# Optimization experiments

Measured on AMD Instinct MI355X. Metric: run time of the kernel, lower is better.

Reference implementation:

```python
import jax, jax.numpy as jnp
import numpy as np

DIM = 1024
NUM_HEADS = 16
HEAD_DIM = DIM // NUM_HEADS
HIDDEN = 2 * DIM  # swiglu hidden


def rotate_half(x):
    x1, x2 = jnp.split(x, 2, axis=-1)
    return jnp.concatenate((-x2, x1), axis=-1)


def setup_inputs() -> dict:
    key = jax.random.key(0)
    ks = jax.random.split(key, 9)
    s = lambda fan_in: 1.0 / np.sqrt(fan_in)
    x = jax.random.normal(ks[0], (4, 2048, DIM), dtype=jnp.float32)
    qkv_w = jax.random.uniform(ks[1], (3 * DIM, DIM), minval=-s(DIM), maxval=s(DIM))
    proj_w = jax.random.uniform(ks[2], (DIM, DIM), minval=-s(DIM), maxval=s(DIM))
    proj_b = jax.random.uniform(ks[3], (DIM,), minval=-s(DIM), maxval=s(DIM))
    w1_w = jax.random.uniform(ks[4], (HIDDEN, DIM), minval=-s(DIM), maxval=s(DIM))
    w1_b = jnp.zeros((HIDDEN,), jnp.float32)
    w2_w = jax.random.uniform(ks[5], (HIDDEN, DIM), minval=-s(DIM), maxval=s(DIM))
    w2_b = jnp.zeros((HIDDEN,), jnp.float32)
    w3_w = jax.random.uniform(ks[6], (DIM, HIDDEN), minval=-s(HIDDEN), maxval=s(HIDDEN))
    w3_b = jnp.zeros((DIM,), jnp.float32)
    return {"x": x, "qkv_w": qkv_w, "proj_w": proj_w, "proj_b": proj_b,
            "w1_w": w1_w, "w1_b": w1_b, "w2_w": w2_w, "w2_b": w2_b,
            "w3_w": w3_w, "w3_b": w3_b}


def reference(x, qkv_w, proj_w, proj_b, w1_w, w1_b, w2_w, w2_b, w3_w, w3_b):
    B, N, C = x.shape
    H, D = NUM_HEADS, HEAD_DIM
    scale = D ** -0.5
    # QKV projection (no bias)
    qkv = jnp.einsum('bnc,fc->bnf', x, qkv_w).reshape(B, N, 3, H, D)
    qkv = jnp.transpose(qkv, (2, 0, 3, 1, 4))  # [3, B, H, N, D]
    q, k, v = qkv[0], qkv[1], qkv[2]
    # Rotary embeddings
    inv_freq = 1.0 / (10000.0 ** (jnp.arange(0, D, 2, dtype=jnp.float32) / D))
    t = jnp.arange(N, dtype=jnp.float32)
    freqs = jnp.einsum('i,j->ij', t, inv_freq)
    emb = jnp.concatenate((freqs, freqs), axis=-1)[None, None]  # [1,1,N,D]
    cos, sin = jnp.cos(emb), jnp.sin(emb)
    q = q * cos + rotate_half(q) * sin
    k = k * cos + rotate_half(k) * sin
    # Attention (non-causal, as in source)
    attn = jnp.einsum('bhnd,bhmd->bhnm', q, k) * scale
    attn = jax.nn.softmax(attn, axis=-1)
    out = jnp.einsum('bhnm,bhmd->bhnd', attn, v)
    out = jnp.transpose(out, (0, 2, 1, 3)).reshape(B, N, C)
    out = jnp.einsum('bnc,fc->bnf', out, proj_w) + proj_b
    # SwiGLU MLP
    x1 = jnp.einsum('bnc,fc->bnf', out, w1_w) + w1_b
    x2 = jnp.einsum('bnc,fc->bnf', out, w2_w) + w2_b
    hidden = jax.nn.silu(x1) * x2
    return jnp.einsum('bnh,fh->bnf', hidden, w3_w) + w3_b
```

## Files before the change

### kernel.cpp

```cpp
#include <hip/hip_runtime.h>
#include <hip/hip_bf16.h>
#include <math.h>


#define SEQ     2048
#define BATCH   4
#define NH      16
#define CDIM    1024
#define MROWS   8192

typedef __bf16 bf16x8 __attribute__((ext_vector_type(8)));
typedef float  floatx4 __attribute__((ext_vector_type(4)));
typedef float  floatx16 __attribute__((ext_vector_type(16)));
typedef unsigned int u32;

__device__ __forceinline__ unsigned short f2bf(float f) {
    __bf16 h = (__bf16)f;
    return __builtin_bit_cast(unsigned short, h);
}
__device__ __forceinline__ float fexp2(float x) {
    float r; asm("v_exp_f32 %0, %1" : "=v"(r) : "v"(x)); return r;
}
__device__ __forceinline__ float frcp(float x) {
    float r; asm("v_rcp_f32 %0, %1" : "=v"(r) : "v"(x)); return r;
}
__device__ __forceinline__ u32 cvtpk(float lo, float hi) {
    u32 w; asm("v_cvt_pk_bf16_f32 %0, %1, %2" : "=v"(w) : "v"(lo), "v"(hi));
    return w;
}
__device__ __forceinline__ floatx4 mfma16(bf16x8 a, bf16x8 b, floatx4 c) {
    return __builtin_amdgcn_mfma_f32_16x16x32_bf16(a, b, c, 0, 0, 0);
}
__device__ __forceinline__ floatx16 mfma32(bf16x8 a, bf16x8 b, floatx16 c) {
    return __builtin_amdgcn_mfma_f32_32x32x16_bf16(a, b, c, 0, 0, 0);
}
__device__ __forceinline__ void gld16(void* lds, const void* g) {
    __builtin_amdgcn_global_load_lds(
        (const __attribute__((address_space(1))) u32*)g,
        (__attribute__((address_space(3))) u32*)lds, 16, 0, 0);
}
__device__ __forceinline__ void wait_vm0_barrier() {
    asm volatile("s_waitcnt vmcnt(0)" ::: "memory");
    __builtin_amdgcn_s_barrier();
    __builtin_amdgcn_sched_barrier(0);
}
__device__ __forceinline__ void raw_barrier() {
    __builtin_amdgcn_s_barrier();
    __builtin_amdgcn_sched_barrier(0);
}

template <int OUTMODE, bool BIAS>
__global__ __launch_bounds__(256) void mgemm(
    const unsigned short* __restrict__ A,
    const unsigned short* __restrict__ B,
    const float* __restrict__ bias,
    void* __restrict__ C, int ldc,
    int K)
{
    __shared__ __align__(16) unsigned short As[2][128 * 32];
    __shared__ __align__(16) unsigned short Bs[2][128 * 32];

    const int tid  = threadIdx.x;
    const int lane = tid & 63;
    const int wave = tid >> 6;
    const int l16  = lane & 15;
    const int quad = lane >> 4;
    const int wm = (wave >> 1) * 64, wn = (wave & 1) * 64;
    const int bm = blockIdx.y, bn = blockIdx.x;

    const unsigned short* Ag = A + (size_t)(bm * 128) * K;
    const unsigned short* Bg = B + (size_t)(bn * 128) * K;

    const int srow0 = wave * 32 + (lane >> 2);
    const int scol  = 8 * ((lane & 3) ^ ((lane >> 3) & 3));
    const unsigned short* gA0 = Ag + (size_t)srow0 * K + scol;
    const unsigned short* gA1 = Ag + (size_t)(srow0 + 16) * K + scol;
    const unsigned short* gB0 = Bg + (size_t)srow0 * K + scol;
    const unsigned short* gB1 = Bg + (size_t)(srow0 + 16) * K + scol;

    auto stage = [&](int b, int kt) {
        gld16(&As[b][(wave * 2 + 0) * 512], gA0 + kt);
        gld16(&As[b][(wave * 2 + 1) * 512], gA1 + kt);
        gld16(&Bs[b][(wave * 2 + 0) * 512], gB0 + kt);
        gld16(&Bs[b][(wave * 2 + 1) * 512], gB1 + kt);
    };

    const int qsw = (quad ^ ((l16 >> 1) & 3)) * 8;

    floatx4 acc[4][4] = {};
    const int NK = K >> 5;

    stage(0, 0);
    wait_vm0_barrier();

    for (int i = 0; i < NK; ++i) {
        const int cur = i & 1;
        if (i + 1 < NK) stage(cur ^ 1, (i + 1) * 32);

        bf16x8 af[4], bfr[4];
        #pragma unroll
        for (int mt = 0; mt < 4; ++mt)
            af[mt] = *(const bf16x8*)&As[cur][(wm + mt * 16 + l16) * 32 + qsw];
        #pragma unroll
        for (int nt = 0; nt < 4; ++nt)
            bfr[nt] = *(const bf16x8*)&Bs[cur][(wn + nt * 16 + l16) * 32 + qsw];
        #pragma unroll
        for (int mt = 0; mt < 4; ++mt)
            #pragma unroll
            for (int nt = 0; nt < 4; ++nt)
                acc[mt][nt] = mfma16(af[mt], bfr[nt], acc[mt][nt]);

        if (i + 1 < NK) wait_vm0_barrier();
        else            raw_barrier();
    }

    #pragma unroll
    for (int nt = 0; nt < 4; ++nt) {
        const int gcol = bn * 128 + wn + nt * 16 + l16;
        const float bv = BIAS ? bias[gcol] : 0.0f;
        #pragma unroll
        for (int mt = 0; mt < 4; ++mt) {
            #pragma unroll
            for (int r = 0; r < 4; ++r) {
                const int grow = bm * 128 + wm + mt * 16 + quad * 4 + r;
                float v = acc[mt][nt][r] + bv;
                if (OUTMODE == 0)
                    ((float*)C)[(size_t)grow * ldc + gcol] = v;
                else
                    ((unsigned short*)C)[(size_t)grow * ldc + gcol] = f2bf(v);
            }
        }
    }
}

__global__ __launch_bounds__(256) void mgemm_glu(
    const unsigned short* __restrict__ A,
    const unsigned short* __restrict__ B1,
    const unsigned short* __restrict__ B2,
    const float* __restrict__ bias1,
    const float* __restrict__ bias2,
    unsigned short* __restrict__ C, int ldc,
    int K)
{
    __shared__ __align__(16) unsigned short As[2][128 * 32];
    __shared__ __align__(16) unsigned short B1s[2][64 * 32];
    __shared__ __align__(16) unsigned short B2s[2][64 * 32];

    const int tid  = threadIdx.x;
    const int lane = tid & 63;
    const int wave = tid >> 6;
    const int l16  = lane & 15;
    const int quad = lane >> 4;
    const int wm = (wave >> 1) * 64, wn = (wave & 1) * 32;
    const int bm = blockIdx.y, bn = blockIdx.x;

    const unsigned short* Ag  = A  + (size_t)(bm * 128) * K;
    const unsigned short* B1g = B1 + (size_t)(bn * 64) * K;
    const unsigned short* B2g = B2 + (size_t)(bn * 64) * K;

    const int arow = wave * 32 + (lane >> 2);
    const int brow = wave * 16 + (lane >> 2);
    const int scol = 8 * ((lane & 3) ^ ((lane >> 3) & 3));
    const unsigned short* gA0 = Ag  + (size_t)arow * K + scol;
    const unsigned short* gA1 = Ag  + (size_t)(arow + 16) * K + scol;
    const unsigned short* gB1 = B1g + (size_t)brow * K + scol;
    const unsigned short* gB2 = B2g + (size_t)brow * K + scol;

    auto stage = [&](int b, int kt) {
        gld16(&As[b][(wave * 2 + 0) * 512], gA0 + kt);
        gld16(&As[b][(wave * 2 + 1) * 512], gA1 + kt);
        gld16(&B1s[b][wave * 512], gB1 + kt);
        gld16(&B2s[b][wave * 512], gB2 + kt);
    };

    const int qsw = (quad ^ ((l16 >> 1) & 3)) * 8;

    floatx4 acc1[4][2] = {};
    floatx4 acc2[4][2] = {};
    const int NK = K >> 5;

    stage(0, 0);
    wait_vm0_barrier();

    for (int i = 0; i < NK; ++i) {
        const int cur = i & 1;
        if (i + 1 < NK) stage(cur ^ 1, (i + 1) * 32);

        bf16x8 af[4], b1f[2], b2f[2];
        #pragma unroll
        for (int mt = 0; mt < 4; ++mt)
            af[mt] = *(const bf16x8*)&As[cur][(wm + mt * 16 + l16) * 32 + qsw];
        #pragma unroll
        for (int nt = 0; nt < 2; ++nt) {
            b1f[nt] = *(const bf16x8*)&B1s[cur][(wn + nt * 16 + l16) * 32 + qsw];
            b2f[nt] = *(const bf16x8*)&B2s[cur][(wn + nt * 16 + l16) * 32 + qsw];
        }
        #pragma unroll
        for (int mt = 0; mt < 4; ++mt)
            #pragma unroll
            for (int nt = 0; nt < 2; ++nt) {
                acc1[mt][nt] = mfma16(af[mt], b1f[nt], acc1[mt][nt]);
                acc2[mt][nt] = mfma16(af[mt], b2f[nt], acc2[mt][nt]);
            }

        if (i + 1 < NK) wait_vm0_barrier();
        else            raw_barrier();
    }

    #pragma unroll
    for (int nt = 0; nt < 2; ++nt) {
        const int gcol = bn * 64 + wn + nt * 16 + l16;
        const float b1 = bias1[gcol];
        const float b2 = bias2[gcol];
        #pragma unroll
        for (int mt = 0; mt < 4; ++mt) {
            #pragma unroll
            for (int r = 0; r < 4; ++r) {
                const int grow = bm * 128 + wm + mt * 16 + quad * 4 + r;
                const float x1 = acc1[mt][nt][r] + b1;
                const float x2 = acc2[mt][nt][r] + b2;
                const float e = fexp2(x1 * -1.44269504088896f);
                const float v = x1 * frcp(1.0f + e) * x2;
                C[(size_t)grow * ldc + gcol] = f2bf(v);
            }
        }
    }
}

#define RD_A(buf, mh)                                                     \
    { _Pragma("unroll") for (int i_ = 0; i_ < 4; ++i_) {                  \
        const int ro_ = (arow + ((mh) * 4 + i_) * 16) * 64;               \
        aF[i_][0] = *(const bf16x8*)&As[buf][ro_ + e0];                   \
        aF[i_][1] = *(const bf16x8*)&As[buf][ro_ + e1]; } }

#define RD_B(buf, nh)                                                     \
    { _Pragma("unroll") for (int n_ = 0; n_ < 2; ++n_) {                  \
        const int ro_ = (brow + ((nh) * 2 + n_) * 16) * 64;               \
        bF[nh][n_][0] = *(const bf16x8*)&Bs[buf][ro_ + e0];               \
        bF[nh][n_][1] = *(const bf16x8*)&Bs[buf][ro_ + e1]; } }

#define DO_MFMA(mh, nh)                                                   \
    { _Pragma("unroll") for (int i_ = 0; i_ < 4; ++i_)                    \
      { _Pragma("unroll") for (int n_ = 0; n_ < 2; ++n_) {                \
        acc[(mh)*4+i_][(nh)*2+n_] =                                       \
            mfma16(aF[i_][0], bF[nh][n_][0], acc[(mh)*4+i_][(nh)*2+n_]);  \
        acc[(mh)*4+i_][(nh)*2+n_] =                                       \
            mfma16(aF[i_][1], bF[nh][n_][1], acc[(mh)*4+i_][(nh)*2+n_]);  \
      } } }

#define PH_ENTER()                                                        \
    __builtin_amdgcn_s_barrier();                                         \
    asm volatile("s_waitcnt lgkmcnt(0)" ::: "memory");                    \
    __builtin_amdgcn_sched_barrier(0);                                    \
    __builtin_amdgcn_s_setprio(1)

#define PH_EXIT() __builtin_amdgcn_s_setprio(0)

__global__ __launch_bounds__(512, 2) void mgemm_qkv(
    const unsigned short* __restrict__ A,
    const unsigned short* __restrict__ B,
    const float* __restrict__ tab,
    unsigned short* __restrict__ Qb,
    unsigned short* __restrict__ Kb,
    unsigned short* __restrict__ Vtb)
{
    __shared__ __align__(16) unsigned short As[2][256 * 64];
    __shared__ __align__(16) unsigned short Bs[2][256 * 64];

    const int tid  = threadIdx.x;
    const int lane = tid & 63;
    const int wave = tid >> 6;
    const int l16  = lane & 15;
    const int quad = lane >> 4;
    const int wr   = wave >> 2;
    const int wc   = wave & 3;
    const int bn = blockIdx.x, bm = blockIdx.y;
    const int K = CDIM;

    const unsigned short* Ag = A + (size_t)(bm * 256) * K;
    const unsigned short* Bg = B + (size_t)(bn * 256) * K;

    const int srow  = lane >> 3;
    const int sgcol = ((lane & 7) ^ srow) * 8;

    auto stA = [&](int buf, int half, int kt) {
        #pragma unroll
        for (int s = 0; s < 2; ++s) {
            const int rbase = half * 128 + (wave * 2 + s) * 8;
            gld16(&As[buf][rbase * 64],
                  Ag + (size_t)(rbase + srow) * K + kt + sgcol);
        }
    };
    auto stB = [&](int buf, int half, int kt) {
        #pragma unroll
        for (int s = 0; s < 2; ++s) {
            const int rbase = half * 128 + (wave * 2 + s) * 8;
            gld16(&Bs[buf][rbase * 64],
                  Bg + (size_t)(rbase + srow) * K + kt + sgcol);
        }
    };

    const int e0 = ((quad)     ^ (l16 & 7)) * 8;
    const int e1 = ((quad + 4) ^ (l16 & 7)) * 8;
    const int arow = wr * 128 + l16;
    const int brow = wc * 64 + l16;

    floatx4 acc[8][4] = {};
    bf16x8 aF[4][2];
    bf16x8 bF[2][2][2];

    stA(0, 0, 0); stA(0, 1, 0); stB(0, 0, 0); stB(0, 1, 0);
    stA(1, 0, 64);
    asm volatile("s_waitcnt vmcnt(2)" ::: "memory");
    __builtin_amdgcn_s_barrier();
    __builtin_amdgcn_sched_barrier(0);

    for (int j = 0; j < 8; ++j) {
        const int k1 = (2 * j + 1) * 64;
        const int k2 = (2 * j + 2) * 64;
        const int k3 = (2 * j + 3) * 64;
        const bool more = (j < 7);

        RD_A(0, 0); RD_B(0, 0);
        stA(1, 1, k1);
        PH_ENTER(); DO_MFMA(0, 0); PH_EXIT();
        __builtin_amdgcn_s_barrier();

        RD_B(0, 1);
        stB(1, 0, k1);
        PH_ENTER(); DO_MFMA(0, 1); PH_EXIT();
        __builtin_amdgcn_s_barrier();

        RD_A(0, 1);
        stB(1, 1, k1);
        PH_ENTER(); DO_MFMA(1, 1); PH_EXIT();
        __builtin_amdgcn_s_barrier();

        if (more) stA(0, 0, k2);
        PH_ENTER(); DO_MFMA(1, 0); PH_EXIT();
        if (more) { asm volatile("s_waitcnt vmcnt(2)" ::: "memory"); }
        else      { asm volatile("s_waitcnt vmcnt(0)" ::: "memory"); }
        __builtin_amdgcn_s_barrier();

        RD_A(1, 0); RD_B(1, 0);
        if (more) stA(0, 1, k2);
        PH_ENTER(); DO_MFMA(0, 0); PH_EXIT();
        __builtin_amdgcn_s_barrier();

        RD_B(1, 1);
        if (more) stB(0, 0, k2);
        PH_ENTER(); DO_MFMA(0, 1); PH_EXIT();
        __builtin_amdgcn_s_barrier();

        RD_A(1, 1);
        if (more) stB(0, 1, k2);
        PH_ENTER(); DO_MFMA(1, 1); PH_EXIT();
        __builtin_amdgcn_s_barrier();

        if (more) stA(1, 0, k3);
        PH_ENTER(); DO_MFMA(1, 0); PH_EXIT();
        if (more) {
            asm volatile("s_waitcnt vmcnt(2)" ::: "memory");
            __builtin_amdgcn_s_barrier();
        }
    }

    const int part = bn >> 2;

    if (part == 2) {
        unsigned short* T = &As[0][0];
        #pragma unroll
        for (int m = 0; m < 8; ++m) {
            __syncthreads();
            #pragma unroll
            for (int n = 0; n < 4; ++n) {
                ushort4 pk;
                pk.x = f2bf(acc[m][n][0]); pk.y = f2bf(acc[m][n][1]);
                pk.z = f2bf(acc[m][n][2]); pk.w = f2bf(acc[m][n][3]);
                *(ushort4*)&T[(wr * 256 + wc * 64 + n * 16 + l16) * 16 + quad * 4] = pk;
            }
            __syncthreads();
            const int wr2 = tid >> 8, col = tid & 255;
            const int grow0 = bm * 256 + wr2 * 128 + m * 16;
            const int b = grow0 >> 11, n0 = grow0 & 2047;
            const int h2 = (bn & 3) * 4 + (col >> 6);
            const int d  = col & 63;
            unsigned short* dst = Vtb +
                ((size_t)(b * NH + h2) * 64 + d) * 2048 + n0;
            const int tb = (wr2 * 256 + col) * 16;
            *(uint4*)dst       = *(const uint4*)&T[tb];
            *(uint4*)(dst + 8) = *(const uint4*)&T[tb + 8];
        }
    } else {
        const float qscale = (part == 0) ? 0.125f * 1.44269504088896f : 1.0f;
        const int h = (bn & 3) * 4 + wc;
        unsigned short* qk = (part == 0) ? Qb : Kb;
        #pragma unroll
        for (int m = 0; m < 8; ++m) {
            #pragma unroll
            for (int r = 0; r < 4; ++r) {
                const int grow = bm * 256 + wr * 128 + m * 16 + quad * 4 + r;
                const int b = grow >> 11, n = grow & 2047;
                unsigned short* dst = qk + ((size_t)(b * NH + h) * 2048 + n) * 64;
                #pragma unroll
                for (int nt = 0; nt < 2; ++nt) {
                    const int i = nt * 16 + l16;
                    const float c  = tab[(n * 32 + i) * 2];
                    const float sn = tab[(n * 32 + i) * 2 + 1];
                    const float x1  = acc[m][nt][r];
                    const float x2v = acc[m][nt + 2][r];
                    dst[i]      = f2bf((x1 * c - x2v * sn) * qscale);
                    dst[i + 32] = f2bf((x2v * c + x1 * sn) * qscale);
                }
            }
        }
    }
}

__global__ __launch_bounds__(256) void attn_mfma(
    const unsigned short* __restrict__ Qb,
    const unsigned short* __restrict__ Kb,
    const unsigned short* __restrict__ Vtb,
    unsigned short* __restrict__ Ob)
{
    const int bh = blockIdx.x;
    const int qt = blockIdx.y;
    const int tid = threadIdx.x;
    const int lane = tid & 63, wave = tid >> 6;
    const int r32 = lane & 31, hi = lane >> 5;
    const int qrow = wave * 32 + r32;

    __shared__ unsigned short QP[128][72];
    __shared__ unsigned short Ks[64][72];
    __shared__ unsigned short Vs[64][72];

    const unsigned short* Qg = Qb + ((size_t)bh * 2048 + qt * 128) * 64;
    const unsigned short* Kg = Kb + (size_t)bh * 2048 * 64;
    const unsigned short* Vg = Vtb + (size_t)bh * 64 * 2048;

    #pragma unroll
    for (int rep = 0; rep < 4; ++rep) {
        const int c = tid + rep * 256;
        const int r = c >> 3, d0 = (c & 7) * 8;
        *(uint4*)&QP[r][d0] = *(const uint4*)(Qg + (size_t)r * 64 + d0);
    }

    const int c0 = tid, c1 = tid + 256;
    const int kr0 = c0 >> 3, kd0 = (c0 & 7) * 8;
    const int kr1 = c1 >> 3, kd1 = (c1 & 7) * 8;

    uint4 ka0 = *(const uint4*)(Kg + (size_t)kr0 * 64 + kd0);
    uint4 ka1 = *(const uint4*)(Kg + (size_t)kr1 * 64 + kd1);
    uint4 va0 = *(const uint4*)(Vg + (size_t)kr0 * 2048 + kd0);
    uint4 va1 = *(const uint4*)(Vg + (size_t)kr1 * 2048 + kd1);

    __syncthreads();

    bf16x8 bq[4];
    #pragma unroll
    for (int f = 0; f < 4; ++f)
        bq[f] = *(const bf16x8*)&QP[qrow][f * 16 + hi * 8];

    floatx16 o0 = {}, o1 = {};
    float l_acc = 0.0f;

    for (int kt = 0; kt < 32; ++kt) {
        __syncthreads();
        *(uint4*)&Ks[kr0][kd0] = ka0;
        *(uint4*)&Ks[kr1][kd1] = ka1;
        *(uint4*)&Vs[kr0][kd0] = va0;
        *(uint4*)&Vs[kr1][kd1] = va1;
        if (kt + 1 < 32) {
            const size_t nb = (size_t)(kt + 1) * 64;
            ka0 = *(const uint4*)(Kg + (nb + kr0) * 64 + kd0);
            ka1 = *(const uint4*)(Kg + (nb + kr1) * 64 + kd1);
            va0 = *(const uint4*)(Vg + (size_t)kr0 * 2048 + nb + kd0);
            va1 = *(const uint4*)(Vg + (size_t)kr1 * 2048 + nb + kd1);
        }
        __syncthreads();

        #pragma unroll
        for (int t = 0; t < 2; ++t) {
            floatx16 s = {};
            #pragma unroll
            for (int f = 0; f < 4; ++f) {
                const bf16x8 ak = *(const bf16x8*)&Ks[t * 32 + r32][f * 16 + hi * 8];
                s = mfma32(ak, bq[f], s);
            }
            float p[16];
            float rs = 0.0f;
            #pragma unroll
            for (int g = 0; g < 16; ++g) { p[g] = fexp2(s[g]); rs += p[g]; }
            l_acc += rs;
            u32 w0 = cvtpk(p[0], p[1]),   w2 = cvtpk(p[4], p[5]);
            u32 w1 = cvtpk(p[2], p[3]),   w3 = cvtpk(p[6], p[7]);
            u32 w4 = cvtpk(p[8], p[9]),   w6 = cvtpk(p[12], p[13]);
            u32 w5 = cvtpk(p[10], p[11]), w7 = cvtpk(p[14], p[15]);
            asm("v_permlane32_swap_b32 %0, %1" : "+v"(w0), "+v"(w2));
            asm("v_permlane32_swap_b32 %0, %1" : "+v"(w1), "+v"(w3));
            asm("v_permlane32_swap_b32 %0, %1" : "+v"(w4), "+v"(w6));
            asm("v_permlane32_swap_b32 %0, %1" : "+v"(w5), "+v"(w7));
            uint4 u0; u0.x = w0; u0.y = w1; u0.z = w2; u0.w = w3;
            uint4 u1; u1.x = w4; u1.y = w5; u1.z = w6; u1.w = w7;
            const bf16x8 bp0 = __builtin_bit_cast(bf16x8, u0);
            const bf16x8 bp1 = __builtin_bit_cast(bf16x8, u1);
            {
                const int f0 = 2 * t, f1 = 2 * t + 1;
                const bf16x8 av00 = *(const bf16x8*)&Vs[r32][f0 * 16 + hi * 8];
                const bf16x8 av01 = *(const bf16x8*)&Vs[32 + r32][f0 * 16 + hi * 8];
                o0 = mfma32(av00, bp0, o0);
                o1 = mfma32(av01, bp0, o1);
                const bf16x8 av10 = *(const bf16x8*)&Vs[r32][f1 * 16 + hi * 8];
                const bf16x8 av11 = *(const bf16x8*)&Vs[32 + r32][f1 * 16 + hi * 8];
                o0 = mfma32(av10, bp1, o0);
                o1 = mfma32(av11, bp1, o1);
            }
        }
    }

    const float l_tot = l_acc + __shfl_xor(l_acc, 32);
    const float inv = 1.0f / l_tot;
    const int b = bh >> 4, h = bh & 15;
    unsigned short* orow = Ob +
        (size_t)(b * SEQ + qt * 128 + qrow) * CDIM + h * 64;
    #pragma unroll
    for (int u = 0; u < 2; ++u) {
        const floatx16 ov = u ? o1 : o0;
        #pragma unroll
        for (int g = 0; g < 4; ++g) {
            ushort4 pk;
            pk.x = f2bf(ov[4 * g + 0] * inv); pk.y = f2bf(ov[4 * g + 1] * inv);
            pk.z = f2bf(ov[4 * g + 2] * inv); pk.w = f2bf(ov[4 * g + 3] * inv);
            *(ushort4*)(orow + u * 32 + 8 * g + 4 * hi) = pk;
        }
    }
}

__global__ __launch_bounds__(256) void cvt_all(
    const float* __restrict__ x,    const float* __restrict__ qkv,
    const float* __restrict__ proj, const float* __restrict__ w1,
    const float* __restrict__ w2,   const float* __restrict__ w3,
    unsigned short* __restrict__ xb,    unsigned short* __restrict__ qkvb,
    unsigned short* __restrict__ projb, unsigned short* __restrict__ w1b,
    unsigned short* __restrict__ w2b,   unsigned short* __restrict__ w3b)
{
    const size_t i = ((size_t)blockIdx.x * 256 + threadIdx.x) * 4;
    const float* src; unsigned short* dst; size_t off;
    if      (i <  8388608) { src = x;    dst = xb;    off = 0; }
    else if (i < 11534336) { src = qkv;  dst = qkvb;  off = 8388608; }
    else if (i < 12582912) { src = proj; dst = projb; off = 11534336; }
    else if (i < 14680064) { src = w1;   dst = w1b;   off = 12582912; }
    else if (i < 16777216) { src = w2;   dst = w2b;   off = 14680064; }
    else                   { src = w3;   dst = w3b;   off = 16777216; }
    const size_t j = i - off;
    const float4 f = *(const float4*)(src + j);
    ushort4 o; o.x = f2bf(f.x); o.y = f2bf(f.y); o.z = f2bf(f.z); o.w = f2bf(f.w);
    *(ushort4*)(dst + j) = o;
}

__global__ __launch_bounds__(256) void rope_table(float* __restrict__ tab)
{
    const int idx = blockIdx.x * 256 + threadIdx.x;
    const int i = idx & 31, n = idx >> 5;
    const double f = (double)n * pow(10000.0, -(double)(2 * i) / 64.0);
    tab[idx * 2]     = (float)cos(f);
    tab[idx * 2 + 1] = (float)sin(f);
}

extern "C" void kernel_launch(void* const* d_in, const int* in_sizes, int n_in,
                              void* d_out, int out_size, void* d_ws, size_t ws_size,
                              hipStream_t stream)
{
    const float* x      = (const float*)d_in[0];
    const float* qkv_w  = (const float*)d_in[1];
    const float* proj_w = (const float*)d_in[2];
    const float* proj_b = (const float*)d_in[3];
    const float* w1_w   = (const float*)d_in[4];
    const float* w1_b   = (const float*)d_in[5];
    const float* w2_w   = (const float*)d_in[6];
    const float* w2_b   = (const float*)d_in[7];
    const float* w3_w   = (const float*)d_in[8];
    const float* w3_b   = (const float*)d_in[9];
    float* out = (float*)d_out;

    char* ws = (char*)d_ws;
    unsigned short* Qb    = (unsigned short*)(ws);
    unsigned short* Kb    = (unsigned short*)(ws + 16777216);
    unsigned short* Vtb   = (unsigned short*)(ws + 33554432);
    unsigned short* Ob    = (unsigned short*)(ws + 50331648);
    unsigned short* out1b = (unsigned short*)(ws + 67108864);
    unsigned short* w1b   = (unsigned short*)(ws + 83886080);
    unsigned short* w2b   = (unsigned short*)(ws + 88080384);
    unsigned short* w3b   = (unsigned short*)(ws + 92274688);
    unsigned short* projb = (unsigned short*)(ws + 96468992);
    unsigned short* xb    = (unsigned short*)(ws + 98566144);
    unsigned short* wqkvb = (unsigned short*)(ws + 115343360);
    float*          tab   = (float*)(ws + 121634816);
    unsigned short* hid   = (unsigned short*)(ws);

    const dim3 blk(256);

    cvt_all<<<dim3(18432), blk, 0, stream>>>(
        x, qkv_w, proj_w, w1_w, w2_w, w3_w,
        xb, wqkvb, projb, w1b, w2b, w3b);
    rope_table<<<dim3(256), blk, 0, stream>>>(tab);

    mgemm_qkv<<<dim3(12, 32), dim3(512), 0, stream>>>(xb, wqkvb, tab, Qb, Kb, Vtb);
    attn_mfma<<<dim3(BATCH * NH, SEQ / 128), blk, 0, stream>>>(Qb, Kb, Vtb, Ob);
    mgemm<1, true><<<dim3(8, 64), blk, 0, stream>>>(
        Ob, projb, proj_b, out1b, CDIM, CDIM);
    mgemm_glu<<<dim3(32, 64), blk, 0, stream>>>(
        out1b, w1b, w2b, w1_b, w2_b, hid, 2048, CDIM);
    mgemm<0, true><<<dim3(8, 64), blk, 0, stream>>>(
        hid, w3b, w3_b, out, CDIM, 2048);
}
```

Before: 443.3 us.

## Port SwiGLU GEMM onto the 256x256 eight-phase pipelined QKV GEMM schedule

Replaces the simple double-buffered 128x64 GLU GEMM with the 512-thread, 256x256-tile eight-phase pipelined kernel already used for the QKV projection. The B tile now interleaves 32-row slices of w1 and w2, so each wave holds matching x1 and x2 accumulators and the SiLU gate can be applied in the epilogue. The intent is better MFMA utilisation and more data reuse per loaded tile. The loop body is shared between both kernels through a macro, and the larger tile needs more registers and LDS per block and leaves a smaller grid.

```diff
diff --git a/kernel.cpp b/kernel.cpp
--- a/kernel.cpp
+++ b/kernel.cpp
@@ -133,100 +133,6 @@
     }
 }
 
-__global__ __launch_bounds__(256) void mgemm_glu(
-    const unsigned short* __restrict__ A,
-    const unsigned short* __restrict__ B1,
-    const unsigned short* __restrict__ B2,
-    const float* __restrict__ bias1,
-    const float* __restrict__ bias2,
-    unsigned short* __restrict__ C, int ldc,
-    int K)
-{
-    __shared__ __align__(16) unsigned short As[2][128 * 32];
-    __shared__ __align__(16) unsigned short B1s[2][64 * 32];
-    __shared__ __align__(16) unsigned short B2s[2][64 * 32];
-
-    const int tid  = threadIdx.x;
-    const int lane = tid & 63;
-    const int wave = tid >> 6;
-    const int l16  = lane & 15;
-    const int quad = lane >> 4;
-    const int wm = (wave >> 1) * 64, wn = (wave & 1) * 32;
-    const int bm = blockIdx.y, bn = blockIdx.x;
-
-    const unsigned short* Ag  = A  + (size_t)(bm * 128) * K;
-    const unsigned short* B1g = B1 + (size_t)(bn * 64) * K;
-    const unsigned short* B2g = B2 + (size_t)(bn * 64) * K;
-
-    const int arow = wave * 32 + (lane >> 2);
-    const int brow = wave * 16 + (lane >> 2);
-    const int scol = 8 * ((lane & 3) ^ ((lane >> 3) & 3));
-    const unsigned short* gA0 = Ag  + (size_t)arow * K + scol;
-    const unsigned short* gA1 = Ag  + (size_t)(arow + 16) * K + scol;
-    const unsigned short* gB1 = B1g + (size_t)brow * K + scol;
-    const unsigned short* gB2 = B2g + (size_t)brow * K + scol;
-
-    auto stage = [&](int b, int kt) {
-        gld16(&As[b][(wave * 2 + 0) * 512], gA0 + kt);
-        gld16(&As[b][(wave * 2 + 1) * 512], gA1 + kt);
-        gld16(&B1s[b][wave * 512], gB1 + kt);
-        gld16(&B2s[b][wave * 512], gB2 + kt);
-    };
-
-    const int qsw = (quad ^ ((l16 >> 1) & 3)) * 8;
-
-    floatx4 acc1[4][2] = {};
-    floatx4 acc2[4][2] = {};
-    const int NK = K >> 5;
-
-    stage(0, 0);
-    wait_vm0_barrier();
-
-    for (int i = 0; i < NK; ++i) {
-        const int cur = i & 1;
-        if (i + 1 < NK) stage(cur ^ 1, (i + 1) * 32);
-
-        bf16x8 af[4], b1f[2], b2f[2];
-        #pragma unroll
-        for (int mt = 0; mt < 4; ++mt)
-            af[mt] = *(const bf16x8*)&As[cur][(wm + mt * 16 + l16) * 32 + qsw];
-        #pragma unroll
-        for (int nt = 0; nt < 2; ++nt) {
-            b1f[nt] = *(const bf16x8*)&B1s[cur][(wn + nt * 16 + l16) * 32 + qsw];
-            b2f[nt] = *(const bf16x8*)&B2s[cur][(wn + nt * 16 + l16) * 32 + qsw];
-        }
-        #pragma unroll
-        for (int mt = 0; mt < 4; ++mt)
-            #pragma unroll
-            for (int nt = 0; nt < 2; ++nt) {
-                acc1[mt][nt] = mfma16(af[mt], b1f[nt], acc1[mt][nt]);
-                acc2[mt][nt] = mfma16(af[mt], b2f[nt], acc2[mt][nt]);
-            }
-
-        if (i + 1 < NK) wait_vm0_barrier();
-        else            raw_barrier();
-    }
-
-    #pragma unroll
-    for (int nt = 0; nt < 2; ++nt) {
-        const int gcol = bn * 64 + wn + nt * 16 + l16;
-        const float b1 = bias1[gcol];
-        const float b2 = bias2[gcol];
-        #pragma unroll
-        for (int mt = 0; mt < 4; ++mt) {
-            #pragma unroll
-            for (int r = 0; r < 4; ++r) {
-                const int grow = bm * 128 + wm + mt * 16 + quad * 4 + r;
-                const float x1 = acc1[mt][nt][r] + b1;
-                const float x2 = acc2[mt][nt][r] + b2;
-                const float e = fexp2(x1 * -1.44269504088896f);
-                const float v = x1 * frcp(1.0f + e) * x2;
-                C[(size_t)grow * ldc + gcol] = f2bf(v);
-            }
-        }
-    }
-}
-
 #define RD_A(buf, mh)                                                     \
     { _Pragma("unroll") for (int i_ = 0; i_ < 4; ++i_) {                  \
         const int ro_ = (arow + ((mh) * 4 + i_) * 16) * 64;               \
@@ -256,13 +162,61 @@
 
 #define PH_EXIT() __builtin_amdgcn_s_setprio(0)
 
-__global__ __launch_bounds__(512, 2) void mgemm_qkv(
+#define EIGHT_PHASE_LOOP()                                                \
+    stA(0, 0, 0); stA(0, 1, 0); stB(0, 0, 0); stB(0, 1, 0);               \
+    stA(1, 0, 64);                                                        \
+    asm volatile("s_waitcnt vmcnt(2)" ::: "memory");                      \
+    __builtin_amdgcn_s_barrier();                                         \
+    __builtin_amdgcn_sched_barrier(0);                                    \
+    for (int j = 0; j < 8; ++j) {                                         \
+        const int k1 = (2 * j + 1) * 64;                                  \
+        const int k2 = (2 * j + 2) * 64;                                  \
+        const int k3 = (2 * j + 3) * 64;                                  \
+        const bool more = (j < 7);                                        \
+        RD_A(0, 0); RD_B(0, 0);                                           \
+        stA(1, 1, k1);                                                    \
+        PH_ENTER(); DO_MFMA(0, 0); PH_EXIT();                             \
+        __builtin_amdgcn_s_barrier();                                     \
+        RD_B(0, 1);                                                       \
+        stB(1, 0, k1);                                                    \
+        PH_ENTER(); DO_MFMA(0, 1); PH_EXIT();                             \
+        __builtin_amdgcn_s_barrier();                                     \
+        RD_A(0, 1);                                                       \
+        stB(1, 1, k1);                                                    \
+        PH_ENTER(); DO_MFMA(1, 1); PH_EXIT();                             \
+        __builtin_amdgcn_s_barrier();                                     \
+        if (more) stA(0, 0, k2);                                          \
+        PH_ENTER(); DO_MFMA(1, 0); PH_EXIT();                             \
+        if (more) { asm volatile("s_waitcnt vmcnt(2)" ::: "memory"); }    \
+        else      { asm volatile("s_waitcnt vmcnt(0)" ::: "memory"); }    \
+        __builtin_amdgcn_s_barrier();                                     \
+        RD_A(1, 0); RD_B(1, 0);                                           \
+        if (more) stA(0, 1, k2);                                          \
+        PH_ENTER(); DO_MFMA(0, 0); PH_EXIT();                             \
+        __builtin_amdgcn_s_barrier();                                     \
+        RD_B(1, 1);                                                       \
+        if (more) stB(0, 0, k2);                                          \
+        PH_ENTER(); DO_MFMA(0, 1); PH_EXIT();                             \
+        __builtin_amdgcn_s_barrier();                                     \
+        RD_A(1, 1);                                                       \
+        if (more) stB(0, 1, k2);                                          \
+        PH_ENTER(); DO_MFMA(1, 1); PH_EXIT();                             \
+        __builtin_amdgcn_s_barrier();                                     \
+        if (more) stA(1, 0, k3);                                          \
+        PH_ENTER(); DO_MFMA(1, 0); PH_EXIT();                             \
+        if (more) {                                                       \
+            asm volatile("s_waitcnt vmcnt(2)" ::: "memory");              \
+            __builtin_amdgcn_s_barrier();                                 \
+        }                                                                 \
+    }
+
+__global__ __launch_bounds__(512, 2) void mgemm_glu(
+    const unsigned short* __restrict__ B1p,
+    const unsigned short* __restrict__ B2p,
     const unsigned short* __restrict__ A,
-    const unsigned short* __restrict__ B,
-    const float* __restrict__ tab,
-    unsigned short* __restrict__ Qb,
-    unsigned short* __restrict__ Kb,
-    unsigned short* __restrict__ Vtb)
+    const float* __restrict__ bias1,
+    const float* __restrict__ bias2,
+    unsigned short* __restrict__ C, int ldc)
 {
     __shared__ __align__(16) unsigned short As[2][256 * 64];
     __shared__ __align__(16) unsigned short Bs[2][256 * 64];
@@ -278,7 +232,6 @@
     const int K = CDIM;
 
     const unsigned short* Ag = A + (size_t)(bm * 256) * K;
-    const unsigned short* Bg = B + (size_t)(bn * 256) * K;
 
     const int srow  = lane >> 3;
     const int sgcol = ((lane & 7) ^ srow) * 8;
@@ -295,8 +248,12 @@
         #pragma unroll
         for (int s = 0; s < 2; ++s) {
             const int rbase = half * 128 + (wave * 2 + s) * 8;
+            const int q = rbase >> 6, r6 = rbase & 63;
+            const unsigned short* src = (r6 < 32)
+                ? B1p + (size_t)(bn * 128 + q * 32 + r6) * K
+                : B2p + (size_t)(bn * 128 + q * 32 + (r6 - 32)) * K;
             gld16(&Bs[buf][rbase * 64],
-                  Bg + (size_t)(rbase + srow) * K + kt + sgcol);
+                  src + (size_t)srow * K + kt + sgcol);
         }
     };
 
@@ -309,61 +266,82 @@
     bf16x8 aF[4][2];
     bf16x8 bF[2][2][2];
 
-    stA(0, 0, 0); stA(0, 1, 0); stB(0, 0, 0); stB(0, 1, 0);
-    stA(1, 0, 64);
-    asm volatile("s_waitcnt vmcnt(2)" ::: "memory");
-    __builtin_amdgcn_s_barrier();
-    __builtin_amdgcn_sched_barrier(0);
-
-    for (int j = 0; j < 8; ++j) {
-        const int k1 = (2 * j + 1) * 64;
-        const int k2 = (2 * j + 2) * 64;
-        const int k3 = (2 * j + 3) * 64;
-        const bool more = (j < 7);
-
-        RD_A(0, 0); RD_B(0, 0);
-        stA(1, 1, k1);
-        PH_ENTER(); DO_MFMA(0, 0); PH_EXIT();
-        __builtin_amdgcn_s_barrier();
-
-        RD_B(0, 1);
-        stB(1, 0, k1);
-        PH_ENTER(); DO_MFMA(0, 1); PH_EXIT();
-        __builtin_amdgcn_s_barrier();
-
-        RD_A(0, 1);
-        stB(1, 1, k1);
-        PH_ENTER(); DO_MFMA(1, 1); PH_EXIT();
-        __builtin_amdgcn_s_barrier();
-
-        if (more) stA(0, 0, k2);
-        PH_ENTER(); DO_MFMA(1, 0); PH_EXIT();
-        if (more) { asm volatile("s_waitcnt vmcnt(2)" ::: "memory"); }
-        else      { asm volatile("s_waitcnt vmcnt(0)" ::: "memory"); }
-        __builtin_amdgcn_s_barrier();
-
-        RD_A(1, 0); RD_B(1, 0);
-        if (more) stA(0, 1, k2);
-        PH_ENTER(); DO_MFMA(0, 0); PH_EXIT();
-        __builtin_amdgcn_s_barrier();
-
-        RD_B(1, 1);
-        if (more) stB(0, 0, k2);
-        PH_ENTER(); DO_MFMA(0, 1); PH_EXIT();
-        __builtin_amdgcn_s_barrier();
-
-        RD_A(1, 1);
-        if (more) stB(0, 1, k2);
-        PH_ENTER(); DO_MFMA(1, 1); PH_EXIT();
-        __builtin_amdgcn_s_barrier();
-
-        if (more) stA(1, 0, k3);
-        PH_ENTER(); DO_MFMA(1, 0); PH_EXIT();
-        if (more) {
-            asm volatile("s_waitcnt vmcnt(2)" ::: "memory");
-            __builtin_amdgcn_s_barrier();
-        }
-    }
+    EIGHT_PHASE_LOOP();
+
+    #pragma unroll
+    for (int nt = 0; nt < 2; ++nt) {
+        const int gcol = bn * 128 + wc * 32 + nt * 16 + l16;
+        const float b1 = bias1[gcol];
+        const float b2 = bias2[gcol];
+        #pragma unroll
+        for (int m = 0; m < 8; ++m) {
+            #pragma unroll
+            for (int r = 0; r < 4; ++r) {
+                const int grow = bm * 256 + wr * 128 + m * 16 + quad * 4 + r;
+                const float x1 = acc[m][nt][r] + b1;
+                const float x2 = acc[m][nt + 2][r] + b2;
+                const float e = fexp2(x1 * -1.44269504088896f);
+                const float v = x1 * frcp(1.0f + e) * x2;
+                C[(size_t)grow * ldc + gcol] = f2bf(v);
+            }
+        }
+    }
+}
+
+__global__ __launch_bounds__(512, 2) void mgemm_qkv(
+    const unsigned short* __restrict__ A,
+    const unsigned short* __restrict__ B,
+    const float* __restrict__ tab,
+    unsigned short* __restrict__ Qb,
+    unsigned short* __restrict__ Kb,
+    unsigned short* __restrict__ Vtb)
+{
+    __shared__ __align__(16) unsigned short As[2][256 * 64];
+    __shared__ __align__(16) unsigned short Bs[2][256 * 64];
+
+    const int tid  = threadIdx.x;
+    const int lane = tid & 63;
+    const int wave = tid >> 6;
+    const int l16  = lane & 15;
+    const int quad = lane >> 4;
+    const int wr   = wave >> 2;
+    const int wc   = wave & 3;
+    const int bn = blockIdx.x, bm = blockIdx.y;
+    const int K = CDIM;
+
+    const unsigned short* Ag = A + (size_t)(bm * 256) * K;
+    const unsigned short* Bg = B + (size_t)(bn * 256) * K;
+
+    const int srow  = lane >> 3;
+    const int sgcol = ((lane & 7) ^ srow) * 8;
+
+    auto stA = [&](int buf, int half, int kt) {
+        #pragma unroll
+        for (int s = 0; s < 2; ++s) {
+            const int rbase = half * 128 + (wave * 2 + s) * 8;
+            gld16(&As[buf][rbase * 64],
+                  Ag + (size_t)(rbase + srow) * K + kt + sgcol);
+        }
+    };
+    auto stB = [&](int buf, int half, int kt) {
+        #pragma unroll
+        for (int s = 0; s < 2; ++s) {
+            const int rbase = half * 128 + (wave * 2 + s) * 8;
+            gld16(&Bs[buf][rbase * 64],
+                  Bg + (size_t)(rbase + srow) * K + kt + sgcol);
+        }
+    };
+
+    const int e0 = ((quad)     ^ (l16 & 7)) * 8;
+    const int e1 = ((quad + 4) ^ (l16 & 7)) * 8;
+    const int arow = wr * 128 + l16;
+    const int brow = wc * 64 + l16;
+
+    floatx4 acc[8][4] = {};
+    bf16x8 aF[4][2];
+    bf16x8 bF[2][2][2];
+
+    EIGHT_PHASE_LOOP();
 
     const int part = bn >> 2;
 
@@ -609,8 +587,8 @@
     attn_mfma<<<dim3(BATCH * NH, SEQ / 128), blk, 0, stream>>>(Qb, Kb, Vtb, Ob);
     mgemm<1, true><<<dim3(8, 64), blk, 0, stream>>>(
         Ob, projb, proj_b, out1b, CDIM, CDIM);
-    mgemm_glu<<<dim3(32, 64), blk, 0, stream>>>(
-        out1b, w1b, w2b, w1_b, w2_b, hid, 2048, CDIM);
+    mgemm_glu<<<dim3(16, 32), dim3(512), 0, stream>>>(
+        w1b, w2b, out1b, w1_b, w2_b, hid, 2048);
     mgemm<0, true><<<dim3(8, 64), blk, 0, stream>>>(
         hid, w3b, w3_b, out, CDIM, 2048);
 }
```

Result: faster. 422.8 us (-4.6%).
